# Performance work log

Hardware: AMD Instinct MI355X
Metric: run time of the kernel (lower is better)

## Reference

```python
import jax, jax.numpy as jnp
import numpy as np

N_NODES = 100000
D_IN = 128
D_OUT = 128
SHAPES = {"r1": 1, "r2": 2, "r3": 3}
N_EDGES = {"r1": 400000, "r2": 300000, "r3": 200000}


def setup_inputs() -> dict:
    key = jax.random.key(0)
    ks = jax.random.split(key, 10)
    inp = {
        "x": jax.random.normal(ks[0], (N_NODES, D_IN), dtype=jnp.float32),
        "A_r1": jax.random.normal(ks[1], (D_IN * 1, D_OUT), dtype=jnp.float32) * 0.05,
        "A_r2": jax.random.normal(ks[2], (D_IN * 2, D_OUT), dtype=jnp.float32) * 0.05,
        "A_r3": jax.random.normal(ks[3], (D_IN * 3, D_OUT), dtype=jnp.float32) * 0.05,
        "C_w": jax.random.normal(ks[4], (D_IN, D_OUT), dtype=jnp.float32) * 0.05,
        "C_b": jax.random.normal(ks[5], (D_OUT,), dtype=jnp.float32) * 0.05,
    }
    for j, (name, shape) in enumerate(SHAPES.items()):
        n = N_EDGES[name] * shape
        inp[f"ei_{name}"] = jax.random.randint(ks[6 + j], (2, n), 0, N_NODES, dtype=jnp.int64)
    return inp


def _edge_type_agg(x, edge_indices, A, shape):
    # edge_indices: [2, n_edges*shape]; row0 = sources, row1 reshaped -> dest per hyperedge
    dest = edge_indices[1].reshape(-1, shape)[:, 0]          # [n_edges]
    gathered = x[edge_indices[0]].reshape(-1, shape * x.shape[1])  # [n_edges, shape*D_IN]
    msg = gathered @ A                                        # [n_edges, D_OUT]
    # 1/count(dest) normalization (torch.unique counts == per-type in-degree)
    deg = jax.ops.segment_sum(jnp.ones_like(dest, dtype=msg.dtype), dest, num_segments=x.shape[0])
    msg = msg / deg[dest][:, None]
    return jax.ops.segment_sum(msg, dest, num_segments=x.shape[0])  # scatter_add


def reference(x, ei_r1, ei_r2, ei_r3, A_r1, A_r2, A_r3, C_w, C_b):
    agg = (_edge_type_agg(x, ei_r1, A_r1, 1)
           + _edge_type_agg(x, ei_r2, A_r2, 2)
           + _edge_type_agg(x, ei_r3, A_r3, 3))
    return x @ C_w + C_b + agg
```

## Files before the change

kernel.cpp:

```cpp
#include <hip/hip_runtime.h>

#define N_NODES 100000
#define D 128

typedef unsigned short u16;
typedef short s16x8 __attribute__((ext_vector_type(8)));
typedef float f32x4 __attribute__((ext_vector_type(4)));
typedef unsigned u32x4 __attribute__((ext_vector_type(4)));


#define ENTS_OFF 2804224L
#define AT_OFF   9204224L
#define XB_OFF   9433600L
#define G_OFF    35033600L

__device__ __forceinline__ u16 f2b(float f) {
    union { float f; unsigned u; } v; v.f = f;
    unsigned r = (v.u + 0x7FFFu + ((v.u >> 16) & 1u)) >> 16;
    return (u16)r;
}
__device__ __forceinline__ unsigned pk(float lo, float hi) {
    return (unsigned)f2b(lo) | ((unsigned)f2b(hi) << 16);
}
__device__ __forceinline__ float blo(unsigned w) { return __uint_as_float(w << 16); }
__device__ __forceinline__ float bhi(unsigned w) { return __uint_as_float(w & 0xFFFF0000u); }


__global__ __launch_bounds__(256) void zero_kernel(int* __restrict__ deg,
                                                   int* __restrict__ flags) {
    int b = blockIdx.x, t = threadIdx.x;
    if (b < 293) {
        int i0 = (b * 256 + t) * 4;
#pragma unroll
        for (int r = 0; r < 4; r++)
            if (i0 + r < 300000) deg[i0 + r] = 0;
    } else {
        if (t < 128) flags[t] = 0;
    }
}


__global__ __launch_bounds__(256) void init_deg(
    const float* __restrict__ x,
    const float* __restrict__ A1, const float* __restrict__ A2,
    const float* __restrict__ A3, const float* __restrict__ Cw,
    const int* __restrict__ e1, const int* __restrict__ e2, const int* __restrict__ e3,
    int ne1, int ne2, int ne3,
    u16* __restrict__ ATb, u16* __restrict__ xb, int* __restrict__ deg) {
    int b = blockIdx.x, t = threadIdx.x;
    if (b < 448) {
        int m = b >> 6;
        int idx = (b & 63) * 256 + t;
        int n = idx >> 7, kk = idx & 127;
        const float* src; int srow;
        if (m == 0)      { src = A1; srow = kk; }
        else if (m < 3)  { src = A2; srow = (m - 1) * 128 + kk; }
        else if (m < 6)  { src = A3; srow = (m - 3) * 128 + kk; }
        else             { src = Cw; srow = kk; }
        ATb[m * 16384 + n * 128 + kk] = f2b(src[(long)srow * 128 + n]);
        return;
    }
    if (b < 6698) {
        int f = (b - 448) * 256 + t;
        int node = f >> 4, j = f & 15;
        const f32x4* xr = (const f32x4*)(x + (long)node * 128 + j * 8);
        f32x4 v0 = __builtin_nontemporal_load(xr);
        f32x4 v1 = __builtin_nontemporal_load(xr + 1);
        u32x4 o;
        o.x = pk(v0.x, v0.y); o.y = pk(v0.z, v0.w);
        o.z = pk(v1.x, v1.y); o.w = pk(v1.z, v1.w);
        *(u32x4*)(xb + (long)node * 128 + j * 8) = o;
        return;
    }
    int g = (b - 6698) * 256 + t;
    if (g < ne1) {
        atomicAdd(&deg[e1[ne1 + g]], 1);
    } else if (g < ne1 + ne2) {
        int e = g - ne1;
        atomicAdd(&deg[N_NODES + e2[ne2 * 2 + e * 2]], 1);
    } else if (g < ne1 + ne2 + ne3) {
        int e = g - ne1 - ne2;
        atomicAdd(&deg[2 * N_NODES + e3[ne3 * 3 + e * 3]], 1);
    }
}


__global__ __launch_bounds__(256) void scan_lookback(
    const int* __restrict__ deg, int* __restrict__ offs, int* __restrict__ cursor,
    int* __restrict__ flags, int n, int nb) {
    __shared__ int s[256];
    __shared__ int bprefix;
    int t = threadIdx.x, bid = blockIdx.x;
    int base = bid * 1024 + t * 4;
    int d1[4], d2[4], v[4], p[4];
#pragma unroll
    for (int r = 0; r < 4; r++) {
        int idx = base + r;
        if (idx < n) {
            d1[r] = deg[idx];
            d2[r] = deg[N_NODES + idx];
            int d3 = deg[2 * N_NODES + idx];
            v[r] = d1[r] + 2 * d2[r] + 3 * d3;
        } else { d1[r] = 0; d2[r] = 0; v[r] = 0; }
    }
    p[0] = 0; p[1] = v[0]; p[2] = v[0] + v[1]; p[3] = v[0] + v[1] + v[2];
    int tsum = p[3] + v[3];
    s[t] = tsum;
    for (int off = 1; off < 256; off <<= 1) {
        __syncthreads();
        int x = (t >= off) ? s[t - off] : 0;
        __syncthreads();
        s[t] += x;
    }
    __syncthreads();
    int total = s[255];
    if (t == 0) {
        int run = 0;
        if (bid == 0) {
            atomicExch(&flags[0], (total << 2) | 2);
        } else {
            atomicExch(&flags[bid], (total << 2) | 1);
            int j = bid - 1;
            while (true) {
                int f = atomicAdd(&flags[j], 0);
                int st = f & 3;
                if (st == 0) continue;
                run += (f >> 2);
                if (st == 2) break;
                j--;
            }
            atomicExch(&flags[bid], ((run + total) << 2) | 2);
        }
        bprefix = run;
        if (bid == nb - 1) offs[n] = run + total;
    }
    __syncthreads();
    int texcl = s[t] - tsum + bprefix;
#pragma unroll
    for (int r = 0; r < 4; r++) {
        int idx = base + r;
        if (idx < n) {
            int val = texcl + p[r];
            offs[idx] = val;
            cursor[idx] = val;
            cursor[N_NODES + idx] = val + d1[r];
            cursor[2 * N_NODES + idx] = val + d1[r] + 2 * d2[r];
        }
    }
}


__global__ __launch_bounds__(256) void scatter_all(
    const int* __restrict__ e1, const int* __restrict__ e2, const int* __restrict__ e3,
    int ne1, int ne2, int ne3, const int* __restrict__ deg,
    int* __restrict__ cursor, int* __restrict__ ents) {
    int g = blockIdx.x * 256 + threadIdx.x;
    if (g < ne1) {
        int dest = e1[ne1 + g];
        int pos = atomicAdd(&cursor[dest], 1);
        ents[pos] = e1[g];
    } else if (g < ne1 + ne2) {
        int e = g - ne1;
        int dest = e2[ne2 * 2 + e * 2];
        int c2 = deg[N_NODES + dest];
        int pos = atomicAdd(&cursor[N_NODES + dest], 1);
        ents[pos]      = e2[e * 2];
        ents[pos + c2] = e2[e * 2 + 1];
    } else if (g < ne1 + ne2 + ne3) {
        int e = g - ne1 - ne2;
        int dest = e3[ne3 * 3 + e * 3];
        int c3 = deg[2 * N_NODES + dest];
        int pos = atomicAdd(&cursor[2 * N_NODES + dest], 1);
        ents[pos]          = e3[e * 3];
        ents[pos + c3]     = e3[e * 3 + 1];
        ents[pos + 2 * c3] = e3[e * 3 + 2];
    }
}


__global__ __launch_bounds__(256) void agg_all(
    const u16* __restrict__ xb, const int* __restrict__ ents,
    const int* __restrict__ offs, const int* __restrict__ deg,
    u16* __restrict__ G) {
    const int lane = threadIdx.x & 63;
    const int wv = __builtin_amdgcn_readfirstlane(threadIdx.x >> 6);
    int wid = blockIdx.x * 4 + wv;
    const int nw = gridDim.x * 4;
    const unsigned cb = (unsigned)lane * 4u;
    const char* xbb = (const char*)xb;

    for (int d = wid; d < N_NODES; d += nw) {
        const int lo = offs[d];
        const int c1 = deg[d], c2 = deg[N_NODES + d], c3 = deg[2 * N_NODES + d];
        float a0l = 0, a0h = 0, a1l = 0, a1h = 0, a2l = 0, a2h = 0;
        float a3l = 0, a3h = 0, a4l = 0, a4h = 0, a5l = 0, a5h = 0;

        int p = 0;
        for (; p + 8 <= c1; p += 8) {
            unsigned w[8];
#pragma unroll
            for (int i = 0; i < 8; i++)
                w[i] = *(const unsigned*)(xbb + (((unsigned)ents[lo + p + i] << 8) + cb));
#pragma unroll
            for (int i = 0; i < 8; i++) { a0l += blo(w[i]); a0h += bhi(w[i]); }
        }
        for (; p < c1; p++) {
            unsigned w = *(const unsigned*)(xbb + (((unsigned)ents[lo + p] << 8) + cb));
            a0l += blo(w); a0h += bhi(w);
        }

        const int o1 = lo + c1;
        p = 0;
        for (; p + 4 <= c2; p += 4) {
            unsigned wa[4], wb[4];
#pragma unroll
            for (int i = 0; i < 4; i++) {
                int e = o1 + p + i;
                wa[i] = *(const unsigned*)(xbb + (((unsigned)ents[e] << 8) + cb));
                wb[i] = *(const unsigned*)(xbb + (((unsigned)ents[e + c2] << 8) + cb));
            }
#pragma unroll
            for (int i = 0; i < 4; i++) {
                a1l += blo(wa[i]); a1h += bhi(wa[i]);
                a2l += blo(wb[i]); a2h += bhi(wb[i]);
            }
        }
        for (; p < c2; p++) {
            int e = o1 + p;
            unsigned wa = *(const unsigned*)(xbb + (((unsigned)ents[e] << 8) + cb));
            unsigned wb = *(const unsigned*)(xbb + (((unsigned)ents[e + c2] << 8) + cb));
            a1l += blo(wa); a1h += bhi(wa);
            a2l += blo(wb); a2h += bhi(wb);
        }

        const int o3 = o1 + 2 * c2;
        p = 0;
        for (; p + 4 <= c3; p += 4) {
            unsigned wa[4], wb[4], wc[4];
#pragma unroll
            for (int i = 0; i < 4; i++) {
                int e = o3 + p + i;
                wa[i] = *(const unsigned*)(xbb + (((unsigned)ents[e] << 8) + cb));
                wb[i] = *(const unsigned*)(xbb + (((unsigned)ents[e + c3] << 8) + cb));
                wc[i] = *(const unsigned*)(xbb + (((unsigned)ents[e + 2 * c3] << 8) + cb));
            }
#pragma unroll
            for (int i = 0; i < 4; i++) {
                a3l += blo(wa[i]); a3h += bhi(wa[i]);
                a4l += blo(wb[i]); a4h += bhi(wb[i]);
                a5l += blo(wc[i]); a5h += bhi(wc[i]);
            }
        }
        for (; p < c3; p++) {
            int e = o3 + p;
            unsigned wa = *(const unsigned*)(xbb + (((unsigned)ents[e] << 8) + cb));
            unsigned wb = *(const unsigned*)(xbb + (((unsigned)ents[e + c3] << 8) + cb));
            unsigned wc = *(const unsigned*)(xbb + (((unsigned)ents[e + 2 * c3] << 8) + cb));
            a3l += blo(wa); a3h += bhi(wa);
            a4l += blo(wb); a4h += bhi(wb);
            a5l += blo(wc); a5h += bhi(wc);
        }

        const float i1 = c1 ? 1.0f / (float)c1 : 0.0f;
        const float i2 = c2 ? 1.0f / (float)c2 : 0.0f;
        const float i3 = c3 ? 1.0f / (float)c3 : 0.0f;
        char* gd = (char*)G + (size_t)d * 1536 + cb;
        __builtin_nontemporal_store(pk(a0l * i1, a0h * i1), (unsigned*)gd);
        __builtin_nontemporal_store(pk(a1l * i2, a1h * i2), (unsigned*)(gd + 256));
        __builtin_nontemporal_store(pk(a2l * i2, a2h * i2), (unsigned*)(gd + 512));
        __builtin_nontemporal_store(pk(a3l * i3, a3h * i3), (unsigned*)(gd + 768));
        __builtin_nontemporal_store(pk(a4l * i3, a4h * i3), (unsigned*)(gd + 1024));
        __builtin_nontemporal_store(pk(a5l * i3, a5h * i3), (unsigned*)(gd + 1280));
    }
}


__global__ __launch_bounds__(256) void gemm_out(
    const u16* __restrict__ G, const u16* __restrict__ xb,
    const u16* __restrict__ AT, const float* __restrict__ Cb,
    float* __restrict__ out) {
    __shared__ __align__(16) float smemf[64 * 132];
    typedef u16 XsT[64][40];
    XsT* Xs = reinterpret_cast<XsT*>(smemf);

    const int t = threadIdx.x;
    const int d0 = blockIdx.x * 64;
    const int lane = t & 63, wv = t >> 6;
    const int nbase = wv * 32, quad = lane >> 4, lrow = lane & 15;

    f32x4 acc[4][2];
#pragma unroll
    for (int mi = 0; mi < 4; mi++)
#pragma unroll
        for (int ni = 0; ni < 2; ni++) acc[mi][ni] = (f32x4)(0.0f);

    for (int s = 0; s < 7; s++) {
#pragma unroll
        for (int i = 0; i < 4; i++) {
            int f = i * 256 + t;
            int row = f >> 4, k8 = f & 15;
            long rs = (d0 + row < N_NODES) ? d0 + row : N_NODES - 1;
            const u16* src = (s < 6) ? (G + rs * 768 + s * 128 + k8 * 8)
                                     : (xb + rs * 128 + k8 * 8);
            u32x4 v = __builtin_nontemporal_load((const u32x4*)src);
            *(u32x4*)&Xs[k8 >> 2][row][(k8 & 3) * 8] = v;
        }
        __syncthreads();
        const u16* B = AT + s * 16384;
        s16x8 bfrag[2][4];
#pragma unroll
        for (int ni = 0; ni < 2; ni++)
#pragma unroll
            for (int c = 0; c < 4; c++)
                bfrag[ni][c] = *(const s16x8*)(B + (nbase + ni * 16 + lrow) * 128 +
                                               c * 32 + quad * 8);
        s16x8 afrag[4][4];
#pragma unroll
        for (int mi = 0; mi < 4; mi++)
#pragma unroll
            for (int c = 0; c < 4; c++)
                afrag[mi][c] = *(const s16x8*)&Xs[c][mi * 16 + lrow][quad * 8];
#pragma unroll
        for (int c = 0; c < 4; c++)
#pragma unroll
            for (int mi = 0; mi < 4; mi++)
#pragma unroll
                for (int ni = 0; ni < 2; ni++)
                    acc[mi][ni] = __builtin_amdgcn_mfma_f32_16x16x32_bf16(
                        afrag[mi][c], bfrag[ni][c], acc[mi][ni], 0, 0, 0);
        __syncthreads();
    }

#pragma unroll
    for (int mi = 0; mi < 4; mi++)
#pragma unroll
        for (int ni = 0; ni < 2; ni++)
#pragma unroll
            for (int reg = 0; reg < 4; reg++) {
                int row = mi * 16 + quad * 4 + reg;
                int colq = nbase + ni * 16 + lrow;
                smemf[row * 132 + colq] = acc[mi][ni][reg];
            }
    __syncthreads();
#pragma unroll
    for (int i = 0; i < 8; i++) {
        int f = i * 256 + t;
        int row = f >> 5;
        int colq = (f & 31) * 4;
        if (d0 + row < N_NODES) {
            f32x4 v = *(const f32x4*)&smemf[row * 132 + colq];
            f32x4 b = *(const f32x4*)&Cb[colq];
            v += b;
            __builtin_nontemporal_store(v, (f32x4*)&out[(long)(d0 + row) * 128 + colq]);
        }
    }
}


extern "C" void kernel_launch(void* const* d_in, const int* in_sizes, int n_in,
                              void* d_out, int out_size, void* d_ws, size_t ws_size,
                              hipStream_t stream) {
    const float* x  = (const float*)d_in[0];
    const float* A1 = (const float*)d_in[1];
    const float* A2 = (const float*)d_in[2];
    const float* A3 = (const float*)d_in[3];
    const float* Cw = (const float*)d_in[4];
    const float* Cb = (const float*)d_in[5];
    const int* e1 = (const int*)d_in[6];
    const int* e2 = (const int*)d_in[7];
    const int* e3 = (const int*)d_in[8];
    float* out = (float*)d_out;

    int* ws = (int*)d_ws;
    int* deg    = ws;
    int* offs   = ws + 300000;
    int* cursor = ws + 400001;
    int* flags  = ws + 700001;
    int* ents   = (int*)((char*)d_ws + ENTS_OFF);
    u16* ATb    = (u16*)((char*)d_ws + AT_OFF);
    u16* xb     = (u16*)((char*)d_ws + XB_OFF);
    u16* G      = (u16*)((char*)d_ws + G_OFF);

    const int NE1 = in_sizes[6] / 2;
    const int NE2 = in_sizes[7] / (2 * 2);
    const int NE3 = in_sizes[8] / (2 * 3);
    const int NET = NE1 + NE2 + NE3;
    const int n = N_NODES;
    const int NB = (n + 1023) / 1024;

    zero_kernel<<<294, 256, 0, stream>>>(deg, flags);
    init_deg<<<448 + 6250 + (NET + 255) / 256, 256, 0, stream>>>(
        x, A1, A2, A3, Cw, e1, e2, e3, NE1, NE2, NE3, ATb, xb, deg);
    scan_lookback<<<NB, 256, 0, stream>>>(deg, offs, cursor, flags, n, NB);
    scatter_all<<<(NET + 255) / 256, 256, 0, stream>>>(e1, e2, e3, NE1, NE2, NE3,
                                                       deg, cursor, ents);
    agg_all<<<2048, 256, 0, stream>>>(xb, ents, offs, deg, G);
    gemm_out<<<(N_NODES + 63) / 64, 256, 0, stream>>>(G, xb, ATb, Cb, out);
}
```

Baseline: 360.9 us.

## Fuse preprocessing kernels into one cooperative kernel with grid syncs

Merges the zeroing, weight/feature conversion and degree counting, prefix scan, and scatter kernels into a single cooperative kernel of 1024 persistent blocks, using grid-wide syncs in place of kernel boundaries. The aim is to remove the launch overhead and inter-kernel gaps of four small launches. In exchange, the work is done in grid-stride loops with fewer resident blocks, and each grid.sync adds its own barrier cost. The lookback scan also now depends on all of its blocks being co-resident.

Measured after the change: 630.9 us. +74.8%, slower.

```diff
diff --git a/kernel.cpp b/kernel.cpp
--- a/kernel.cpp
+++ b/kernel.cpp
@@ -1,4 +1,7 @@
 #include <hip/hip_runtime.h>
+#include <hip/hip_cooperative_groups.h>
+
+namespace cg = cooperative_groups;
 
 #define N_NODES 100000
 #define D 128
@@ -26,154 +29,146 @@
 __device__ __forceinline__ float bhi(unsigned w) { return __uint_as_float(w & 0xFFFF0000u); }
 
 
-__global__ __launch_bounds__(256) void zero_kernel(int* __restrict__ deg,
-                                                   int* __restrict__ flags) {
-    int b = blockIdx.x, t = threadIdx.x;
-    if (b < 293) {
-        int i0 = (b * 256 + t) * 4;
-#pragma unroll
-        for (int r = 0; r < 4; r++)
-            if (i0 + r < 300000) deg[i0 + r] = 0;
-    } else {
-        if (t < 128) flags[t] = 0;
-    }
-}
-
-
-__global__ __launch_bounds__(256) void init_deg(
+__global__ __launch_bounds__(256, 4) void pre_all(
     const float* __restrict__ x,
     const float* __restrict__ A1, const float* __restrict__ A2,
     const float* __restrict__ A3, const float* __restrict__ Cw,
     const int* __restrict__ e1, const int* __restrict__ e2, const int* __restrict__ e3,
     int ne1, int ne2, int ne3,
-    u16* __restrict__ ATb, u16* __restrict__ xb, int* __restrict__ deg) {
-    int b = blockIdx.x, t = threadIdx.x;
-    if (b < 448) {
-        int m = b >> 6;
-        int idx = (b & 63) * 256 + t;
-        int n = idx >> 7, kk = idx & 127;
-        const float* src; int srow;
-        if (m == 0)      { src = A1; srow = kk; }
-        else if (m < 3)  { src = A2; srow = (m - 1) * 128 + kk; }
-        else if (m < 6)  { src = A3; srow = (m - 3) * 128 + kk; }
-        else             { src = Cw; srow = kk; }
-        ATb[m * 16384 + n * 128 + kk] = f2b(src[(long)srow * 128 + n]);
-        return;
-    }
-    if (b < 6698) {
-        int f = (b - 448) * 256 + t;
-        int node = f >> 4, j = f & 15;
-        const f32x4* xr = (const f32x4*)(x + (long)node * 128 + j * 8);
-        f32x4 v0 = __builtin_nontemporal_load(xr);
-        f32x4 v1 = __builtin_nontemporal_load(xr + 1);
-        u32x4 o;
-        o.x = pk(v0.x, v0.y); o.y = pk(v0.z, v0.w);
-        o.z = pk(v1.x, v1.y); o.w = pk(v1.z, v1.w);
-        *(u32x4*)(xb + (long)node * 128 + j * 8) = o;
-        return;
-    }
-    int g = (b - 6698) * 256 + t;
-    if (g < ne1) {
-        atomicAdd(&deg[e1[ne1 + g]], 1);
-    } else if (g < ne1 + ne2) {
-        int e = g - ne1;
-        atomicAdd(&deg[N_NODES + e2[ne2 * 2 + e * 2]], 1);
-    } else if (g < ne1 + ne2 + ne3) {
-        int e = g - ne1 - ne2;
-        atomicAdd(&deg[2 * N_NODES + e3[ne3 * 3 + e * 3]], 1);
-    }
-}
-
-
-__global__ __launch_bounds__(256) void scan_lookback(
-    const int* __restrict__ deg, int* __restrict__ offs, int* __restrict__ cursor,
-    int* __restrict__ flags, int n, int nb) {
+    u16* __restrict__ ATb, u16* __restrict__ xb, int* __restrict__ deg,
+    int* __restrict__ offs, int* __restrict__ cursor, int* __restrict__ flags,
+    int* __restrict__ ents) {
+    cg::grid_group grid = cg::this_grid();
     __shared__ int s[256];
     __shared__ int bprefix;
-    int t = threadIdx.x, bid = blockIdx.x;
-    int base = bid * 1024 + t * 4;
-    int d1[4], d2[4], v[4], p[4];
-#pragma unroll
-    for (int r = 0; r < 4; r++) {
-        int idx = base + r;
-        if (idx < n) {
-            d1[r] = deg[idx];
-            d2[r] = deg[N_NODES + idx];
-            int d3 = deg[2 * N_NODES + idx];
-            v[r] = d1[r] + 2 * d2[r] + 3 * d3;
-        } else { d1[r] = 0; d2[r] = 0; v[r] = 0; }
-    }
-    p[0] = 0; p[1] = v[0]; p[2] = v[0] + v[1]; p[3] = v[0] + v[1] + v[2];
-    int tsum = p[3] + v[3];
-    s[t] = tsum;
-    for (int off = 1; off < 256; off <<= 1) {
+    const int b = blockIdx.x, t = threadIdx.x;
+    const int nblk = gridDim.x;
+    const int net = ne1 + ne2 + ne3;
+
+    for (int i = b * 256 + t; i < 300000; i += nblk * 256) deg[i] = 0;
+    if (b == 0 && t < 128) flags[t] = 0;
+    grid.sync();
+
+    const int nvb = 448 + 6250 + (net + 255) / 256;
+    for (int vb = b; vb < nvb; vb += nblk) {
+        if (vb < 448) {
+            int m = vb >> 6;
+            int idx = (vb & 63) * 256 + t;
+            int n = idx >> 7, kk = idx & 127;
+            const float* src; int srow;
+            if (m == 0)      { src = A1; srow = kk; }
+            else if (m < 3)  { src = A2; srow = (m - 1) * 128 + kk; }
+            else if (m < 6)  { src = A3; srow = (m - 3) * 128 + kk; }
+            else             { src = Cw; srow = kk; }
+            ATb[m * 16384 + n * 128 + kk] = f2b(src[(long)srow * 128 + n]);
+        } else if (vb < 6698) {
+            int f = (vb - 448) * 256 + t;
+            int node = f >> 4, j = f & 15;
+            const f32x4* xr = (const f32x4*)(x + (long)node * 128 + j * 8);
+            f32x4 v0 = __builtin_nontemporal_load(xr);
+            f32x4 v1 = __builtin_nontemporal_load(xr + 1);
+            u32x4 o;
+            o.x = pk(v0.x, v0.y); o.y = pk(v0.z, v0.w);
+            o.z = pk(v1.x, v1.y); o.w = pk(v1.z, v1.w);
+            *(u32x4*)(xb + (long)node * 128 + j * 8) = o;
+        } else {
+            int g = (vb - 6698) * 256 + t;
+            if (g < ne1) {
+                atomicAdd(&deg[e1[ne1 + g]], 1);
+            } else if (g < ne1 + ne2) {
+                int e = g - ne1;
+                atomicAdd(&deg[N_NODES + e2[ne2 * 2 + e * 2]], 1);
+            } else if (g < net) {
+                int e = g - ne1 - ne2;
+                atomicAdd(&deg[2 * N_NODES + e3[ne3 * 3 + e * 3]], 1);
+            }
+        }
+    }
+    grid.sync();
+
+    const int n = N_NODES;
+    const int nb = (n + 1023) / 1024;
+    if (b < nb) {
+        int base = b * 1024 + t * 4;
+        int d1[4], d2[4], v[4], p[4];
+#pragma unroll
+        for (int r = 0; r < 4; r++) {
+            int idx = base + r;
+            if (idx < n) {
+                d1[r] = deg[idx];
+                d2[r] = deg[N_NODES + idx];
+                int d3 = deg[2 * N_NODES + idx];
+                v[r] = d1[r] + 2 * d2[r] + 3 * d3;
+            } else { d1[r] = 0; d2[r] = 0; v[r] = 0; }
+        }
+        p[0] = 0; p[1] = v[0]; p[2] = v[0] + v[1]; p[3] = v[0] + v[1] + v[2];
+        int tsum = p[3] + v[3];
+        s[t] = tsum;
+        for (int off = 1; off < 256; off <<= 1) {
+            __syncthreads();
+            int xx = (t >= off) ? s[t - off] : 0;
+            __syncthreads();
+            s[t] += xx;
+        }
         __syncthreads();
-        int x = (t >= off) ? s[t - off] : 0;
+        int total = s[255];
+        if (t == 0) {
+            int run = 0;
+            if (b == 0) {
+                atomicExch(&flags[0], (total << 2) | 2);
+            } else {
+                atomicExch(&flags[b], (total << 2) | 1);
+                int j = b - 1;
+                while (true) {
+                    int f = atomicAdd(&flags[j], 0);
+                    int st = f & 3;
+                    if (st == 0) continue;
+                    run += (f >> 2);
+                    if (st == 2) break;
+                    j--;
+                }
+                atomicExch(&flags[b], ((run + total) << 2) | 2);
+            }
+            bprefix = run;
+            if (b == nb - 1) offs[n] = run + total;
+        }
         __syncthreads();
-        s[t] += x;
-    }
-    __syncthreads();
-    int total = s[255];
-    if (t == 0) {
-        int run = 0;
-        if (bid == 0) {
-            atomicExch(&flags[0], (total << 2) | 2);
+        int texcl = s[t] - tsum + bprefix;
+#pragma unroll
+        for (int r = 0; r < 4; r++) {
+            int idx = base + r;
+            if (idx < n) {
+                int val = texcl + p[r];
+                offs[idx] = val;
+                cursor[idx] = val;
+                cursor[N_NODES + idx] = val + d1[r];
+                cursor[2 * N_NODES + idx] = val + d1[r] + 2 * d2[r];
+            }
+        }
+    }
+    grid.sync();
+
+    for (int g = b * 256 + t; g < net; g += nblk * 256) {
+        if (g < ne1) {
+            int dest = e1[ne1 + g];
+            int pos = atomicAdd(&cursor[dest], 1);
+            ents[pos] = e1[g];
+        } else if (g < ne1 + ne2) {
+            int e = g - ne1;
+            int dest = e2[ne2 * 2 + e * 2];
+            int c2 = deg[N_NODES + dest];
+            int pos = atomicAdd(&cursor[N_NODES + dest], 1);
+            ents[pos]      = e2[e * 2];
+            ents[pos + c2] = e2[e * 2 + 1];
         } else {
-            atomicExch(&flags[bid], (total << 2) | 1);
-            int j = bid - 1;
-            while (true) {
-                int f = atomicAdd(&flags[j], 0);
-                int st = f & 3;
-                if (st == 0) continue;
-                run += (f >> 2);
-                if (st == 2) break;
-                j--;
-            }
-            atomicExch(&flags[bid], ((run + total) << 2) | 2);
-        }
-        bprefix = run;
-        if (bid == nb - 1) offs[n] = run + total;
-    }
-    __syncthreads();
-    int texcl = s[t] - tsum + bprefix;
-#pragma unroll
-    for (int r = 0; r < 4; r++) {
-        int idx = base + r;
-        if (idx < n) {
-            int val = texcl + p[r];
-            offs[idx] = val;
-            cursor[idx] = val;
-            cursor[N_NODES + idx] = val + d1[r];
-            cursor[2 * N_NODES + idx] = val + d1[r] + 2 * d2[r];
-        }
-    }
-}
-
-
-__global__ __launch_bounds__(256) void scatter_all(
-    const int* __restrict__ e1, const int* __restrict__ e2, const int* __restrict__ e3,
-    int ne1, int ne2, int ne3, const int* __restrict__ deg,
-    int* __restrict__ cursor, int* __restrict__ ents) {
-    int g = blockIdx.x * 256 + threadIdx.x;
-    if (g < ne1) {
-        int dest = e1[ne1 + g];
-        int pos = atomicAdd(&cursor[dest], 1);
-        ents[pos] = e1[g];
-    } else if (g < ne1 + ne2) {
-        int e = g - ne1;
-        int dest = e2[ne2 * 2 + e * 2];
-        int c2 = deg[N_NODES + dest];
-        int pos = atomicAdd(&cursor[N_NODES + dest], 1);
-        ents[pos]      = e2[e * 2];
-        ents[pos + c2] = e2[e * 2 + 1];
-    } else if (g < ne1 + ne2 + ne3) {
-        int e = g - ne1 - ne2;
-        int dest = e3[ne3 * 3 + e * 3];
-        int c3 = deg[2 * N_NODES + dest];
-        int pos = atomicAdd(&cursor[2 * N_NODES + dest], 1);
-        ents[pos]          = e3[e * 3];
-        ents[pos + c3]     = e3[e * 3 + 1];
-        ents[pos + 2 * c3] = e3[e * 3 + 2];
+            int e = g - ne1 - ne2;
+            int dest = e3[ne3 * 3 + e * 3];
+            int c3 = deg[2 * N_NODES + dest];
+            int pos = atomicAdd(&cursor[2 * N_NODES + dest], 1);
+            ents[pos]          = e3[e * 3];
+            ents[pos + c3]     = e3[e * 3 + 1];
+            ents[pos + 2 * c3] = e3[e * 3 + 2];
+        }
     }
 }
 
@@ -381,19 +376,14 @@
     u16* xb     = (u16*)((char*)d_ws + XB_OFF);
     u16* G      = (u16*)((char*)d_ws + G_OFF);
 
-    const int NE1 = in_sizes[6] / 2;
-    const int NE2 = in_sizes[7] / (2 * 2);
-    const int NE3 = in_sizes[8] / (2 * 3);
-    const int NET = NE1 + NE2 + NE3;
-    const int n = N_NODES;
-    const int NB = (n + 1023) / 1024;
-
-    zero_kernel<<<294, 256, 0, stream>>>(deg, flags);
-    init_deg<<<448 + 6250 + (NET + 255) / 256, 256, 0, stream>>>(
-        x, A1, A2, A3, Cw, e1, e2, e3, NE1, NE2, NE3, ATb, xb, deg);
-    scan_lookback<<<NB, 256, 0, stream>>>(deg, offs, cursor, flags, n, NB);
-    scatter_all<<<(NET + 255) / 256, 256, 0, stream>>>(e1, e2, e3, NE1, NE2, NE3,
-                                                       deg, cursor, ents);
+    int ne1 = in_sizes[6] / 2;
+    int ne2 = in_sizes[7] / (2 * 2);
+    int ne3 = in_sizes[8] / (2 * 3);
+
+    void* args[] = {&x, &A1, &A2, &A3, &Cw, &e1, &e2, &e3,
+                    &ne1, &ne2, &ne3, &ATb, &xb, &deg, &offs, &cursor, &flags, &ents};
+    hipLaunchCooperativeKernel((const void*)pre_all, dim3(1024), dim3(256),
+                               args, 0, stream);
     agg_all<<<2048, 256, 0, stream>>>(xb, ents, offs, deg, G);
     gemm_out<<<(N_NODES + 63) / 64, 256, 0, stream>>>(G, xb, ATb, Cb, out);
 }
```

## Rebalance prep kernels and double-buffer LDS staging in output GEMM

Applied to the files above, without the earlier changes.

Replaces the zero kernel with a memset, moves the weight transpose into the scan launch and the x-to-bf16 conversion into the scatter launch, so the lightly loaded scan and scatter phases get extra parallel work. The output GEMM now double-buffers its LDS tiles, prefetching the next K-slice into registers while computing the current one, which removes one barrier per step. This costs more LDS per block, which may lower occupancy, and reorders the flag and offset workspace so one memset covers both.

Measured after the change: 356.7 us. About the same (-1.2%).

```diff
diff --git a/kernel.cpp b/kernel.cpp
--- a/kernel.cpp
+++ b/kernel.cpp
@@ -26,53 +26,10 @@
 __device__ __forceinline__ float bhi(unsigned w) { return __uint_as_float(w & 0xFFFF0000u); }
 
 
-__global__ __launch_bounds__(256) void zero_kernel(int* __restrict__ deg,
-                                                   int* __restrict__ flags) {
-    int b = blockIdx.x, t = threadIdx.x;
-    if (b < 293) {
-        int i0 = (b * 256 + t) * 4;
-#pragma unroll
-        for (int r = 0; r < 4; r++)
-            if (i0 + r < 300000) deg[i0 + r] = 0;
-    } else {
-        if (t < 128) flags[t] = 0;
-    }
-}
-
-
-__global__ __launch_bounds__(256) void init_deg(
-    const float* __restrict__ x,
-    const float* __restrict__ A1, const float* __restrict__ A2,
-    const float* __restrict__ A3, const float* __restrict__ Cw,
+__global__ __launch_bounds__(256) void deg_all(
     const int* __restrict__ e1, const int* __restrict__ e2, const int* __restrict__ e3,
-    int ne1, int ne2, int ne3,
-    u16* __restrict__ ATb, u16* __restrict__ xb, int* __restrict__ deg) {
-    int b = blockIdx.x, t = threadIdx.x;
-    if (b < 448) {
-        int m = b >> 6;
-        int idx = (b & 63) * 256 + t;
-        int n = idx >> 7, kk = idx & 127;
-        const float* src; int srow;
-        if (m == 0)      { src = A1; srow = kk; }
-        else if (m < 3)  { src = A2; srow = (m - 1) * 128 + kk; }
-        else if (m < 6)  { src = A3; srow = (m - 3) * 128 + kk; }
-        else             { src = Cw; srow = kk; }
-        ATb[m * 16384 + n * 128 + kk] = f2b(src[(long)srow * 128 + n]);
-        return;
-    }
-    if (b < 6698) {
-        int f = (b - 448) * 256 + t;
-        int node = f >> 4, j = f & 15;
-        const f32x4* xr = (const f32x4*)(x + (long)node * 128 + j * 8);
-        f32x4 v0 = __builtin_nontemporal_load(xr);
-        f32x4 v1 = __builtin_nontemporal_load(xr + 1);
-        u32x4 o;
-        o.x = pk(v0.x, v0.y); o.y = pk(v0.z, v0.w);
-        o.z = pk(v1.x, v1.y); o.w = pk(v1.z, v1.w);
-        *(u32x4*)(xb + (long)node * 128 + j * 8) = o;
-        return;
-    }
-    int g = (b - 6698) * 256 + t;
+    int ne1, int ne2, int ne3, int* __restrict__ deg) {
+    int g = blockIdx.x * 256 + threadIdx.x;
     if (g < ne1) {
         atomicAdd(&deg[e1[ne1 + g]], 1);
     } else if (g < ne1 + ne2) {
@@ -85,12 +42,28 @@
 }
 
 
-__global__ __launch_bounds__(256) void scan_lookback(
+__global__ __launch_bounds__(256) void scan_atb(
     const int* __restrict__ deg, int* __restrict__ offs, int* __restrict__ cursor,
-    int* __restrict__ flags, int n, int nb) {
+    int* __restrict__ flags,
+    const float* __restrict__ A1, const float* __restrict__ A2,
+    const float* __restrict__ A3, const float* __restrict__ Cw,
+    u16* __restrict__ ATb, int n, int nb) {
+    const int t = threadIdx.x, bid = blockIdx.x;
+    if (bid >= nb) {
+        int mb = bid - nb;
+        int m = mb >> 6;
+        int idx = (mb & 63) * 256 + t;
+        int nn = idx >> 7, kk = idx & 127;
+        const float* src; int srow;
+        if (m == 0)      { src = A1; srow = kk; }
+        else if (m < 3)  { src = A2; srow = (m - 1) * 128 + kk; }
+        else if (m < 6)  { src = A3; srow = (m - 3) * 128 + kk; }
+        else             { src = Cw; srow = kk; }
+        ATb[m * 16384 + nn * 128 + kk] = f2b(src[(long)srow * 128 + nn]);
+        return;
+    }
     __shared__ int s[256];
     __shared__ int bprefix;
-    int t = threadIdx.x, bid = blockIdx.x;
     int base = bid * 1024 + t * 4;
     int d1[4], d2[4], v[4], p[4];
 #pragma unroll
@@ -150,11 +123,25 @@
 }
 
 
-__global__ __launch_bounds__(256) void scatter_all(
+__global__ __launch_bounds__(256) void scatter_xconv(
+    const float* __restrict__ x, u16* __restrict__ xb,
     const int* __restrict__ e1, const int* __restrict__ e2, const int* __restrict__ e3,
     int ne1, int ne2, int ne3, const int* __restrict__ deg,
     int* __restrict__ cursor, int* __restrict__ ents) {
-    int g = blockIdx.x * 256 + threadIdx.x;
+    int b = blockIdx.x, t = threadIdx.x;
+    if (b < 6250) {
+        int f = b * 256 + t;
+        int node = f >> 4, j = f & 15;
+        const f32x4* xr = (const f32x4*)(x + (long)node * 128 + j * 8);
+        f32x4 v0 = __builtin_nontemporal_load(xr);
+        f32x4 v1 = __builtin_nontemporal_load(xr + 1);
+        u32x4 o;
+        o.x = pk(v0.x, v0.y); o.y = pk(v0.z, v0.w);
+        o.z = pk(v1.x, v1.y); o.w = pk(v1.z, v1.w);
+        *(u32x4*)(xb + (long)node * 128 + j * 8) = o;
+        return;
+    }
+    int g = (b - 6250) * 256 + t;
     if (g < ne1) {
         int dest = e1[ne1 + g];
         int pos = atomicAdd(&cursor[dest], 1);
@@ -279,9 +266,7 @@
     const u16* __restrict__ G, const u16* __restrict__ xb,
     const u16* __restrict__ AT, const float* __restrict__ Cb,
     float* __restrict__ out) {
-    __shared__ __align__(16) float smemf[64 * 132];
-    typedef u16 XsT[64][40];
-    XsT* Xs = reinterpret_cast<XsT*>(smemf);
+    __shared__ __align__(16) u16 Xs[2][4][64][40];
 
     const int t = threadIdx.x;
     const int d0 = blockIdx.x * 64;
@@ -294,18 +279,34 @@
 #pragma unroll
         for (int ni = 0; ni < 2; ni++) acc[mi][ni] = (f32x4)(0.0f);
 
+    u32x4 stg[4];
+#pragma unroll
+    for (int i = 0; i < 4; i++) {
+        int f = i * 256 + t;
+        int row = f >> 4, k8 = f & 15;
+        long rs = (d0 + row < N_NODES) ? d0 + row : N_NODES - 1;
+        stg[i] = __builtin_nontemporal_load((const u32x4*)(G + rs * 768 + k8 * 8));
+    }
+#pragma unroll
+    for (int i = 0; i < 4; i++) {
+        int f = i * 256 + t;
+        int row = f >> 4, k8 = f & 15;
+        *(u32x4*)&Xs[0][k8 >> 2][row][(k8 & 3) * 8] = stg[i];
+    }
+    __syncthreads();
+
     for (int s = 0; s < 7; s++) {
-#pragma unroll
-        for (int i = 0; i < 4; i++) {
-            int f = i * 256 + t;
-            int row = f >> 4, k8 = f & 15;
-            long rs = (d0 + row < N_NODES) ? d0 + row : N_NODES - 1;
-            const u16* src = (s < 6) ? (G + rs * 768 + s * 128 + k8 * 8)
-                                     : (xb + rs * 128 + k8 * 8);
-            u32x4 v = __builtin_nontemporal_load((const u32x4*)src);
-            *(u32x4*)&Xs[k8 >> 2][row][(k8 & 3) * 8] = v;
-        }
-        __syncthreads();
+        if (s < 6) {
+#pragma unroll
+            for (int i = 0; i < 4; i++) {
+                int f = i * 256 + t;
+                int row = f >> 4, k8 = f & 15;
+                long rs = (d0 + row < N_NODES) ? d0 + row : N_NODES - 1;
+                const u16* src = (s + 1 < 6) ? (G + rs * 768 + (s + 1) * 128 + k8 * 8)
+                                             : (xb + rs * 128 + k8 * 8);
+                stg[i] = __builtin_nontemporal_load((const u32x4*)src);
+            }
+        }
         const u16* B = AT + s * 16384;
         s16x8 bfrag[2][4];
 #pragma unroll
@@ -314,23 +315,32 @@
             for (int c = 0; c < 4; c++)
                 bfrag[ni][c] = *(const s16x8*)(B + (nbase + ni * 16 + lrow) * 128 +
                                                c * 32 + quad * 8);
-        s16x8 afrag[4][4];
-#pragma unroll
-        for (int mi = 0; mi < 4; mi++)
-#pragma unroll
-            for (int c = 0; c < 4; c++)
-                afrag[mi][c] = *(const s16x8*)&Xs[c][mi * 16 + lrow][quad * 8];
-#pragma unroll
-        for (int c = 0; c < 4; c++)
+        const int cur = s & 1;
+#pragma unroll
+        for (int c = 0; c < 4; c++) {
+            s16x8 a[4];
+#pragma unroll
+            for (int mi = 0; mi < 4; mi++)
+                a[mi] = *(const s16x8*)&Xs[cur][c][mi * 16 + lrow][quad * 8];
 #pragma unroll
             for (int mi = 0; mi < 4; mi++)
 #pragma unroll
                 for (int ni = 0; ni < 2; ni++)
                     acc[mi][ni] = __builtin_amdgcn_mfma_f32_16x16x32_bf16(
-                        afrag[mi][c], bfrag[ni][c], acc[mi][ni], 0, 0, 0);
+                        a[mi], bfrag[ni][c], acc[mi][ni], 0, 0, 0);
+        }
+        if (s < 6) {
+#pragma unroll
+            for (int i = 0; i < 4; i++) {
+                int f = i * 256 + t;
+                int row = f >> 4, k8 = f & 15;
+                *(u32x4*)&Xs[cur ^ 1][k8 >> 2][row][(k8 & 3) * 8] = stg[i];
+            }
+        }
         __syncthreads();
     }
 
+    float* smf = (float*)&Xs[0][0][0][0];
 #pragma unroll
     for (int mi = 0; mi < 4; mi++)
 #pragma unroll
@@ -339,7 +349,7 @@
             for (int reg = 0; reg < 4; reg++) {
                 int row = mi * 16 + quad * 4 + reg;
                 int colq = nbase + ni * 16 + lrow;
-                smemf[row * 132 + colq] = acc[mi][ni][reg];
+                smf[row * 132 + colq] = acc[mi][ni][reg];
             }
     __syncthreads();
 #pragma unroll
@@ -348,7 +358,7 @@
         int row = f >> 5;
         int colq = (f & 31) * 4;
         if (d0 + row < N_NODES) {
-            f32x4 v = *(const f32x4*)&smemf[row * 132 + colq];
+            f32x4 v = *(const f32x4*)&smf[row * 132 + colq];
             f32x4 b = *(const f32x4*)&Cb[colq];
             v += b;
             __builtin_nontemporal_store(v, (f32x4*)&out[(long)(d0 + row) * 128 + colq]);
@@ -373,9 +383,9 @@
 
     int* ws = (int*)d_ws;
     int* deg    = ws;
-    int* offs   = ws + 300000;
-    int* cursor = ws + 400001;
-    int* flags  = ws + 700001;
+    int* flags  = ws + 300000;
+    int* offs   = ws + 300128;
+    int* cursor = ws + 400129;
     int* ents   = (int*)((char*)d_ws + ENTS_OFF);
     u16* ATb    = (u16*)((char*)d_ws + AT_OFF);
     u16* xb     = (u16*)((char*)d_ws + XB_OFF);
@@ -388,12 +398,12 @@
     const int n = N_NODES;
     const int NB = (n + 1023) / 1024;
 
-    zero_kernel<<<294, 256, 0, stream>>>(deg, flags);
-    init_deg<<<448 + 6250 + (NET + 255) / 256, 256, 0, stream>>>(
-        x, A1, A2, A3, Cw, e1, e2, e3, NE1, NE2, NE3, ATb, xb, deg);
-    scan_lookback<<<NB, 256, 0, stream>>>(deg, offs, cursor, flags, n, NB);
-    scatter_all<<<(NET + 255) / 256, 256, 0, stream>>>(e1, e2, e3, NE1, NE2, NE3,
-                                                       deg, cursor, ents);
+    hipMemsetAsync(deg, 0, (300000 + 128) * sizeof(int), stream);
+    deg_all<<<(NET + 255) / 256, 256, 0, stream>>>(e1, e2, e3, NE1, NE2, NE3, deg);
+    scan_atb<<<NB + 448, 256, 0, stream>>>(deg, offs, cursor, flags,
+                                           A1, A2, A3, Cw, ATb, n, NB);
+    scatter_xconv<<<6250 + (NET + 255) / 256, 256, 0, stream>>>(
+        x, xb, e1, e2, e3, NE1, NE2, NE3, deg, cursor, ents);
     agg_all<<<2048, 256, 0, stream>>>(xb, ents, offs, deg, G);
     gemm_out<<<(N_NODES + 63) / 64, 256, 0, stream>>>(G, xb, ATb, Cb, out);
 }
```
